# Optimization experiments

Measured on AMD Instinct MI355X. Metric: run time of the kernel, lower is better.

Reference implementation:

```python
import jax, jax.numpy as jnp
import numpy as np

VOCAB = 128000
DIM = 1024
B, S = 8, 2048


def setup_inputs() -> dict:
    key = jax.random.key(0)
    k1, k2, k3, k4 = jax.random.split(key, 4)
    input = jax.random.randint(k1, (B, S), 0, VOCAB, dtype=jnp.int64)
    # uint8-valued codes stored as int32 (values in [0, 256))
    qweight = jax.random.randint(k2, (VOCAB, DIM), 0, 256, dtype=jnp.int32)
    scales = jax.random.uniform(k3, (VOCAB,), dtype=jnp.float32) * 0.02
    zeros = jax.random.uniform(k4, (VOCAB,), dtype=jnp.float32) * 255.0
    return {"input": input, "qweight": qweight, "scales": scales, "zeros": zeros}


def reference(input, qweight, scales, zeros):
    # Faithful to the torch module: dequantize the FULL table, then gather rows.
    # weight[r, d] = (q[r, d] - zero[r]) * scale[r]
    weight = (qweight.astype(jnp.float32) - zeros[:, None]) * scales[:, None]  # [V, D]
    return weight[input]  # [B, S, D] gather (padding_idx=None -> plain embedding lookup)
```

## Files before the change

### kernel.cpp

```cpp
#include <hip/hip_runtime.h>


constexpr int DIM = 1024;

typedef int   int4v   __attribute__((ext_vector_type(4)));
typedef float float4v __attribute__((ext_vector_type(4)));

__global__ __launch_bounds__(256) void qembed_kernel(
    const int*   __restrict__ input,
    const int*   __restrict__ qweight,
    const float* __restrict__ scales,
    const float* __restrict__ zeros,
    float*       __restrict__ out,
    int ntok)
{
    const int tok = blockIdx.x;
    if (tok >= ntok) return;

    const int row = input[tok];
    const float scale = scales[row];
    const float zero  = zeros[row];

    const int4v* qrow = reinterpret_cast<const int4v*>(qweight + (size_t)row * DIM);
    float4v*     orow = reinterpret_cast<float4v*>(out + (size_t)tok * DIM);

    const int t = threadIdx.x;
    int4v q = qrow[t];
    float4v o;
    o.x = ((float)q.x - zero) * scale;
    o.y = ((float)q.y - zero) * scale;
    o.z = ((float)q.z - zero) * scale;
    o.w = ((float)q.w - zero) * scale;
    __builtin_nontemporal_store(o, orow + t);
}

extern "C" void kernel_launch(void* const* d_in, const int* in_sizes, int n_in,
                              void* d_out, int out_size, void* d_ws, size_t ws_size,
                              hipStream_t stream) {
    const int*   input   = (const int*)d_in[0];
    const int*   qweight = (const int*)d_in[1];
    const float* scales  = (const float*)d_in[2];
    const float* zeros   = (const float*)d_in[3];
    float*       out     = (float*)d_out;

    const int ntok = in_sizes[0];
    dim3 grid(ntok);
    dim3 block(256);
    qembed_kernel<<<grid, block, 0, stream>>>(input, qweight, scales, zeros, out, ntok);
}
```

Baseline: 25.46 us.

## Use grid-stride persistent blocks with prefetch of next token's row metadata

Replaces the one-block-per-token launch with a fixed grid of 2048 blocks that stride over tokens. Each iteration prefetches the next token's index, scale and zero before processing the current row, so the dependent index lookup latency overlaps with the current load and store. This cuts block launch overhead but gives fewer blocks in flight and adds a serial dependency chain per block.

```diff
diff --git a/kernel.cpp b/kernel.cpp
--- a/kernel.cpp
+++ b/kernel.cpp
@@ -14,24 +14,39 @@
     float*       __restrict__ out,
     int ntok)
 {
-    const int tok = blockIdx.x;
+    const int t = threadIdx.x;
+    const int G = gridDim.x;
+    int tok = blockIdx.x;
     if (tok >= ntok) return;
 
-    const int row = input[tok];
-    const float scale = scales[row];
-    const float zero  = zeros[row];
+    int   row = input[tok];
+    float sc  = scales[row];
+    float zp  = zeros[row];
 
-    const int4v* qrow = reinterpret_cast<const int4v*>(qweight + (size_t)row * DIM);
-    float4v*     orow = reinterpret_cast<float4v*>(out + (size_t)tok * DIM);
+    for (;;) {
+        const int  ntk  = tok + G;
+        const bool more = ntk < ntok;
+        int   nrow = 0;
+        float nsc = 0.f, nzp = 0.f;
+        if (more) {
+            nrow = input[ntk];
+            nsc  = scales[nrow];
+            nzp  = zeros[nrow];
+        }
 
-    const int t = threadIdx.x;
-    int4v q = qrow[t];
-    float4v o;
-    o.x = ((float)q.x - zero) * scale;
-    o.y = ((float)q.y - zero) * scale;
-    o.z = ((float)q.z - zero) * scale;
-    o.w = ((float)q.w - zero) * scale;
-    __builtin_nontemporal_store(o, orow + t);
+        const int4v* qrow = reinterpret_cast<const int4v*>(qweight + (size_t)row * DIM);
+        float4v*     orow = reinterpret_cast<float4v*>(out + (size_t)tok * DIM);
+        int4v q = qrow[t];
+        float4v o;
+        o.x = ((float)q.x - zp) * sc;
+        o.y = ((float)q.y - zp) * sc;
+        o.z = ((float)q.z - zp) * sc;
+        o.w = ((float)q.w - zp) * sc;
+        __builtin_nontemporal_store(o, orow + t);
+
+        if (!more) break;
+        tok = ntk; row = nrow; sc = nsc; zp = nzp;
+    }
 }
 
 extern "C" void kernel_launch(void* const* d_in, const int* in_sizes, int n_in,
@@ -44,7 +59,8 @@
     float*       out     = (float*)d_out;
 
     const int ntok = in_sizes[0];
-    dim3 grid(ntok);
+    const int nblocks = 2048;
+    dim3 grid(nblocks);
     dim3 block(256);
     qembed_kernel<<<grid, block, 0, stream>>>(input, qweight, scales, zeros, out, ntok);
 }
```

Measured after the change: 26.57 us. +4.4%, slower.
